# Kernel optimization log

Measured on AMD Instinct MI355X. Metric: run time of the kernel, lower is better.

The kernel has to match this reference:

```python
import jax, jax.numpy as jnp
import numpy as np

B, L, D, H = 4, 1024, 256, 8
TEMP = float(np.sqrt(D))
EPS_SM = 1e-6
EPS_LN = 1e-5


def setup_inputs() -> dict:
    key = jax.random.key(0)
    ks = jax.random.split(key, 8)
    std = float(np.sqrt(2.0 / (D * 2)))
    return {
        "q": jax.random.normal(ks[0], (B, L, D), jnp.float32),
        "mask": jax.random.randint(ks[1], (B, L, L), 0, 2, jnp.int32),
        "k": jax.random.normal(ks[2], (B, L, D), jnp.float32),
        "v": jax.random.normal(ks[3], (B, L, D), jnp.float32),
        "w_qs": jax.random.normal(ks[4], (H * D, D), jnp.float32) * std,
        "w_ks": jax.random.normal(ks[5], (H * D, D), jnp.float32) * std,
        "w_vs": jax.random.normal(ks[6], (H * D, D), jnp.float32) * std,
        "fc_w": jax.random.normal(ks[7], (D, H * D), jnp.float32) * float(np.sqrt(2.0 / (D + H * D))),
        "fc_b": jnp.zeros((D,), jnp.float32),
        "ln_g": jnp.ones((D,), jnp.float32),
        "ln_b": jnp.zeros((D,), jnp.float32),
    }


def masked_softmax(x, m):
    # repo's layers.masked_softmax: clamp, mask-mul, stable exp, mask-mul, normalize
    x = jnp.clip(x, -15.0, 15.0) * m
    e = jnp.exp(x - jnp.max(x, axis=-1, keepdims=True)) * m
    return e / (jnp.sum(e, axis=-1, keepdims=True) + EPS_SM)


def reference(q, mask, k, v, w_qs, w_ks, w_vs, fc_w, fc_b, ln_g, ln_b):
    residual = q
    m = mask.astype(q.dtype)[:, None, :, :]          # [B,1,Lq,Lk]
    # projections to per-head full-dim: [B,L,H,D]
    qh = (q @ w_qs.T).reshape(B, L, H, D)
    kh = (k @ w_ks.T).reshape(B, L, H, D)
    vh = (v @ w_vs.T).reshape(B, L, H, D)
    scores = jnp.einsum("bqhd,bkhd->bhqk", qh, kh) / TEMP   # [B,H,Lq,Lk]
    attn = masked_softmax(scores, m)
    out = jnp.einsum("bhqk,bkhd->bqhd", attn, vh).reshape(B, L, H * D)
    out = out @ fc_w.T + fc_b                         # [B,L,D]
    out = out + residual
    mu = jnp.mean(out, axis=-1, keepdims=True)
    var = jnp.var(out, axis=-1, keepdims=True)
    out = (out - mu) / jnp.sqrt(var + EPS_LN) * ln_g + ln_b
    # match torch attn layout: [H*B, Lq, Lk] (head-major)
    attn_hb = jnp.transpose(attn, (1, 0, 2, 3)).reshape(H * B, L, L)
    return out, attn_hb
```

## Files before the change

kernel.cpp:

```cpp
#include <hip/hip_runtime.h>
#include <cstdint>
#include <math.h>

#define Bsz 4
#define Lsz 1024
#define Dsz 256
#define Hsz 8
#define HD  2048
#define NROWS (Bsz*Lsz)
#define INV_TEMP 0.0625f

typedef __attribute__((ext_vector_type(8))) short bf16x8;
typedef __attribute__((ext_vector_type(4))) float f32x4;

__device__ inline unsigned short f2bf(float f) {
    union { float f; unsigned u; } x; x.f = f;
    unsigned r = x.u + 0x7fffu + ((x.u >> 16) & 1u);
    return (unsigned short)(r >> 16);
}
__device__ inline float bf2f(unsigned short u) {
    union { unsigned u; float f; } x; x.u = (unsigned)u << 16; return x.f;
}

#define GBL(p) ((const __attribute__((address_space(1))) unsigned int*)(p))
#define LDS(p) ((__attribute__((address_space(3))) unsigned int*)(p))

template<int N> __device__ __forceinline__ void vmw() {
    if constexpr (N == 0)       asm volatile("s_waitcnt vmcnt(0)"  ::: "memory");
    else if constexpr (N == 4)  asm volatile("s_waitcnt vmcnt(4)"  ::: "memory");
    else if constexpr (N == 6)  asm volatile("s_waitcnt vmcnt(6)"  ::: "memory");
    else if constexpr (N == 10) asm volatile("s_waitcnt vmcnt(10)" ::: "memory");
    else if constexpr (N == 14) asm volatile("s_waitcnt vmcnt(14)" ::: "memory");
    else static_assert(N == 0, "unsupported vmcnt literal");
}

template <int TMv, int TNv, typename OutT, int EPI, int MINW, bool FUSE,
          int GX, int GY, int GZ>
__global__ __launch_bounds__(256, MINW) void gemm_bt(
    const unsigned short* __restrict__ A, const unsigned short* __restrict__ Bm,
    OutT* __restrict__ C,
    int K, int lda, int ldb, int ldc, int inner,
    long long sA1, long long sA2, long long sB1, long long sB2,
    long long sC1, long long sC2, float alpha,
    const unsigned char* __restrict__ maskb, long long sM2,
    const float* __restrict__ invs, long long sI1, long long sI2,
    float* __restrict__ aux,
    const unsigned short* __restrict__ A2, const unsigned short* __restrict__ B2,
    unsigned short* __restrict__ C2)
{
    constexpr int WMv = TMv / 2, WNv = TNv / 2;
    constexpr int IT = TMv / 32, JT = TNv / 32;
    constexpr int APASS = TMv / 32, NPASS = (TMv + TNv) / 32;
    constexpr int TILE = (TMv + TNv) * 64;
    constexpr int G = GX * GY * GZ;
    static_assert(G % 8 == 0, "bijective XCD swizzle needs G%8==0");
    static_assert(NPASS == 6 || NPASS == 10, "vmcnt literals assume NPASS in {6,10}");
    static_assert(EPI != 1 || TNv == 128, "EPI=1 rowsum shfl assumes 4 segs");
    static_assert(TMv * (TNv + 4) * 4 <= 2 * TILE * 2, "epilogue LDS overflow");

    const int z  = blockIdx.z;

    const int lid = blockIdx.x + GX * (blockIdx.y + GY * blockIdx.z);
    const int nid = (lid & 7) * (G >> 3) + (lid >> 3);
    int mx = nid % GX;
    const int t1g = nid / GX;
    int my = t1g % GY;
    const int zz = t1g / GY;

    if constexpr (FUSE) {
        if (zz >= 2) {
            const int idx = my * 64 + mx;
            if (idx >= 256) return;
            mx = idx & 31; my = idx >> 5;
            const int b = zz - 2;
            A   = A2;
            Bm  = B2 + (size_t)b * ((size_t)Lsz * Dsz);
            C   = (OutT*)(C2 + (size_t)b * ((size_t)HD * Lsz));
            ldc = Lsz;
        } else {
            A  += (size_t)zz * sA2;
            Bm += (size_t)zz * sB2;
            C  += (size_t)zz * sC2;
        }
    } else {
        const int i1 = zz / inner;
        const int i2 = zz % inner;
        A  += (size_t)i1 * sA1 + (size_t)i2 * sA2;
        Bm += (size_t)i1 * sB1 + (size_t)i2 * sB2;
        C  += (size_t)i1 * sC1 + (size_t)i2 * sC2;
        if (EPI == 1) { maskb += (size_t)i2 * sM2; aux += (size_t)zz * Lsz; }
        if (EPI == 2) { invs  += (size_t)i1 * sI1 + (size_t)i2 * sI2; aux += (size_t)zz * Lsz * Lsz; }
    }
    (void)z;

    __shared__ unsigned short S[2 * TILE];

    const int t    = threadIdx.x;
    const int lane = t & 63;
    const int w    = t >> 6;
    const int wm   = w & 1;
    const int wn   = w >> 1;
    const int m0   = mx * TMv;
    const int n0   = my * TNv;

    const int rA = t >> 3;
    const int ch = ((t & 7) ^ (rA & 7)) * 8;
    const unsigned short* gA = A  + (size_t)(m0 + rA) * lda + ch;
    const unsigned short* gB = Bm + (size_t)(n0 + rA) * ldb + ch;

    const int fr = lane & 15;
    const int q  = lane >> 4;

    f32x4 acc[IT][JT];
#pragma unroll
    for (int i = 0; i < IT; ++i)
#pragma unroll
        for (int j = 0; j < JT; ++j) acc[i][j] = (f32x4){0.f, 0.f, 0.f, 0.f};

    auto stage = [&](unsigned short* Sb, int k0) {
#pragma unroll
        for (int p = 0; p < NPASS; ++p) {
            const unsigned short* src = (p < APASS)
                ? (gA + (size_t)p * 32 * lda + k0)
                : (gB + (size_t)(p - APASS) * 32 * ldb + k0);
            __builtin_amdgcn_global_load_lds(GBL(src), LDS(Sb + p * 2048 + t * 8), 16, 0, 0);
        }
    };
    auto kstep = [&](const unsigned short* As) {
        const unsigned short* Bs = As + TMv * 64;
#pragma unroll
        for (int ks = 0; ks < 2; ++ks) {
            const int slot = ((ks * 4 + q) ^ (fr & 7)) * 8;
            bf16x8 a[IT], b[JT];
#pragma unroll
            for (int i = 0; i < IT; ++i)
                a[i] = *(const bf16x8*)(As + (wm * WMv + i * 16 + fr) * 64 + slot);
#pragma unroll
            for (int j = 0; j < JT; ++j)
                b[j] = *(const bf16x8*)(Bs + (wn * WNv + j * 16 + fr) * 64 + slot);
#pragma unroll
            for (int i = 0; i < IT; ++i)
#pragma unroll
                for (int j = 0; j < JT; ++j)
                    acc[i][j] = __builtin_amdgcn_mfma_f32_16x16x32_bf16(a[i], b[j], acc[i][j], 0, 0, 0);
        }
    };

    const int nk = K >> 6;

    float ainv[EPI == 2 ? (TMv / 32) : 1];
    if constexpr (EPI == 2) {
        const int rsub = lane >> 3;
#pragma unroll
        for (int pass = 0; pass < TMv / 32; ++pass)
            ainv[pass] = 1.0f / (invs[m0 + w * (TMv / 4) + pass * 8 + rsub] + 1e-6f);
        vmw<0>();
    }

    stage(S, 0);

    for (int kt = 0; kt < nk; ++kt) {
        if (kt + 1 < nk) stage(S + ((kt + 1) & 1) * TILE, (kt + 1) << 6);

        if constexpr (EPI == 2) {
            if (kt + 1 < nk) { if (kt >= 1) vmw<NPASS + 4>(); else vmw<NPASS>(); }
            else             { if (kt >= 1) vmw<4>();         else vmw<0>(); }
        } else {
            if (kt + 1 < nk) vmw<NPASS>(); else vmw<0>();
        }
        __builtin_amdgcn_s_barrier();

        kstep(S + (kt & 1) * TILE);

        if constexpr (EPI == 2) {
            const unsigned short* As = S + (kt & 1) * TILE;
            const int chunk = lane & 7;
            const int rsub  = lane >> 3;
#pragma unroll
            for (int pass = 0; pass < TMv / 32; ++pass) {
                const int row = w * (TMv / 4) + pass * 8 + rsub;
                const uint4 u = *(const uint4*)(As + row * 64 + ((chunk ^ (row & 7)) * 8));
                const float iv = ainv[pass];
                float4 lo, hi;
                lo.x = bf2f((unsigned short)(u.x & 0xffff)) * iv; lo.y = bf2f((unsigned short)(u.x >> 16)) * iv;
                lo.z = bf2f((unsigned short)(u.y & 0xffff)) * iv; lo.w = bf2f((unsigned short)(u.y >> 16)) * iv;
                hi.x = bf2f((unsigned short)(u.z & 0xffff)) * iv; hi.y = bf2f((unsigned short)(u.z >> 16)) * iv;
                hi.z = bf2f((unsigned short)(u.w & 0xffff)) * iv; hi.w = bf2f((unsigned short)(u.w >> 16)) * iv;
                float* op = aux + (size_t)(m0 + row) * Lsz + (kt << 6) + chunk * 8;
                *(float4*)op = lo;
                *(float4*)(op + 4) = hi;
            }
        }

        asm volatile("s_waitcnt lgkmcnt(0)" ::: "memory");
        __builtin_amdgcn_s_barrier();
    }

    {
        float* Lf = (float*)S;
        constexpr int LP = TNv + 4;
#pragma unroll
        for (int i = 0; i < IT; ++i)
#pragma unroll
            for (int j = 0; j < JT; ++j) {
                const int col = wn * WNv + j * 16 + fr;
#pragma unroll
                for (int r = 0; r < 4; ++r) {
                    const int row = wm * WMv + i * 16 + q * 4 + r;
                    Lf[row * LP + col] = acc[i][j][r] * alpha;
                }
            }
        __syncthreads();

        constexpr int SEGS = TNv / 32;
        constexpr int RPI  = 256 / SEGS;
#pragma unroll
        for (int it2 = 0; it2 < TMv / RPI; ++it2) {
            const int row = it2 * RPI + t / SEGS;
            const int c0  = (t % SEGS) * 32;
            const float* src = Lf + row * LP + c0;

            if constexpr (EPI == 0 && sizeof(OutT) == 4) {
                float* dst = (float*)C + (size_t)(m0 + row) * ldc + n0 + c0;
#pragma unroll
                for (int v4 = 0; v4 < 8; ++v4)
                    *(f32x4*)(dst + v4 * 4) = *(const f32x4*)(src + v4 * 4);
            } else if constexpr (EPI == 0) {
                unsigned short* dst = (unsigned short*)C + (size_t)(m0 + row) * ldc + n0 + c0;
#pragma unroll
                for (int v8 = 0; v8 < 4; ++v8) {
                    bf16x8 o;
#pragma unroll
                    for (int e = 0; e < 8; ++e) o[e] = (short)f2bf(src[v8 * 8 + e]);
                    *(bf16x8*)(dst + v8 * 8) = o;
                }
            } else if constexpr (EPI == 1) {
                unsigned short* dst = (unsigned short*)C + (size_t)(m0 + row) * ldc + n0 + c0;
                const unsigned char* mrow = maskb + (size_t)(m0 + row) * Lsz + n0 + c0;
                unsigned char mloc[32];
                *(uint4*)mloc        = *(const uint4*)mrow;
                *(uint4*)(mloc + 16) = *(const uint4*)(mrow + 16);
                float rsum = 0.f;
#pragma unroll
                for (int v8 = 0; v8 < 4; ++v8) {
                    bf16x8 o;
#pragma unroll
                    for (int e = 0; e < 8; ++e) {
                        const float m = (float)mloc[v8 * 8 + e];
                        float vv = fminf(fmaxf(src[v8 * 8 + e], -15.f), 15.f) * m;
                        vv = __expf(vv) * m;
                        const unsigned short us = f2bf(vv);
                        o[e] = (short)us;
                        rsum += bf2f(us);
                    }
                    *(bf16x8*)(dst + v8 * 8) = o;
                }
                rsum += __shfl_xor(rsum, 1, 64);
                rsum += __shfl_xor(rsum, 2, 64);
                if ((t & 3) == 0) atomicAdd(&aux[m0 + row], rsum);
            } else {
                unsigned short* dst = (unsigned short*)C + (size_t)(m0 + row) * ldc + n0 + c0;
                const float iv = 1.0f / (invs[m0 + row] + 1e-6f);
#pragma unroll
                for (int v8 = 0; v8 < 4; ++v8) {
                    bf16x8 o;
#pragma unroll
                    for (int e = 0; e < 8; ++e) o[e] = (short)f2bf(src[v8 * 8 + e] * iv);
                    *(bf16x8*)(dst + v8 * 8) = o;
                }
            }
        }
    }
}

__global__ __launch_bounds__(256) void cast_all(
    const float* __restrict__ q, const float* __restrict__ k, const float* __restrict__ v,
    const float* __restrict__ wq, const float* __restrict__ wk, const float* __restrict__ wv,
    const float* __restrict__ fw, const int* __restrict__ mask,
    unsigned short* __restrict__ qb, unsigned short* __restrict__ kb, unsigned short* __restrict__ vb,
    unsigned short* __restrict__ wqb, unsigned short* __restrict__ wkb, unsigned short* __restrict__ wvb,
    unsigned short* __restrict__ fwb, unsigned char* __restrict__ mb,
    float* __restrict__ rs)
{
    const int gid = blockIdx.x * 256 + threadIdx.x;
    const int NQ = 262144;
    const int NW = 131072;
    const int NF = 3 * NQ + 4 * NW;
    const int NM = 1048576;
    if (gid >= NF) {
        const int off = gid - NF;
        if (off >= NM) {
            const int ri = off - NM;
            if (ri < 8192) ((float4*)rs)[ri] = (float4){0.f, 0.f, 0.f, 0.f};
            return;
        }
        const int4 mi = ((const int4*)mask)[off];
        uchar4 o;
        o.x = mi.x ? 1 : 0;
        o.y = mi.y ? 1 : 0;
        o.z = mi.z ? 1 : 0;
        o.w = mi.w ? 1 : 0;
        ((uchar4*)mb)[off] = o;
        return;
    }
    const float* src; unsigned short* dst; int off;
    if      (gid < NQ)            { src = q;  dst = qb;  off = gid; }
    else if (gid < 2 * NQ)        { src = k;  dst = kb;  off = gid - NQ; }
    else if (gid < 3 * NQ)        { src = v;  dst = vb;  off = gid - 2 * NQ; }
    else if (gid < 3 * NQ + NW)   { src = wq; dst = wqb; off = gid - 3 * NQ; }
    else if (gid < 3 * NQ + 2*NW) { src = wk; dst = wkb; off = gid - 3 * NQ - NW; }
    else if (gid < 3 * NQ + 3*NW) { src = wv; dst = wvb; off = gid - 3 * NQ - 2 * NW; }
    else                          { src = fw; dst = fwb; off = gid - 3 * NQ - 3 * NW; }
    float4 f = ((const float4*)src)[off];
    ushort4 o;
    o.x = f2bf(f.x); o.y = f2bf(f.y); o.z = f2bf(f.z); o.w = f2bf(f.w);
    ((ushort4*)dst)[off] = o;
}

__global__ __launch_bounds__(256) void ln_kernel(const float* __restrict__ gout,
                                                 const float* __restrict__ qin,
                                                 const float* __restrict__ fc_b,
                                                 const float* __restrict__ ln_g,
                                                 const float* __restrict__ ln_b,
                                                 float* __restrict__ out)
{
    const int row = blockIdx.x;
    const int t = threadIdx.x;
    const size_t idx = (size_t)row * Dsz + t;
    const size_t P = (size_t)NROWS * Dsz;
    const float val = gout[idx] + gout[idx + P] + gout[idx + 2 * P] + gout[idx + 3 * P]
                    + fc_b[t] + qin[idx];

    __shared__ float red[4];
    float s = val;
#pragma unroll
    for (int o = 32; o > 0; o >>= 1) s += __shfl_down(s, o, 64);
    const int lane = t & 63, w = t >> 6;
    if (lane == 0) red[w] = s;
    __syncthreads();
    const float mu = (red[0] + red[1] + red[2] + red[3]) * (1.0f / Dsz);
    __syncthreads();

    float d = val - mu;
    float s2 = d * d;
#pragma unroll
    for (int o = 32; o > 0; o >>= 1) s2 += __shfl_down(s2, o, 64);
    if (lane == 0) red[w] = s2;
    __syncthreads();
    const float var = (red[0] + red[1] + red[2] + red[3]) * (1.0f / Dsz);

    out[idx] = d * rsqrtf(var + 1e-5f) * ln_g[t] + ln_b[t];
}

extern "C" void kernel_launch(void* const* d_in, const int* in_sizes, int n_in,
                              void* d_out, int out_size, void* d_ws, size_t ws_size,
                              hipStream_t stream)
{
    const float* q    = (const float*)d_in[0];
    const int*   mask = (const int*)d_in[1];
    const float* k    = (const float*)d_in[2];
    const float* v    = (const float*)d_in[3];
    const float* w_qs = (const float*)d_in[4];
    const float* w_ks = (const float*)d_in[5];
    const float* w_vs = (const float*)d_in[6];
    const float* fc_w = (const float*)d_in[7];
    const float* fc_b = (const float*)d_in[8];
    const float* ln_g = (const float*)d_in[9];
    const float* ln_b = (const float*)d_in[10];

    float* out  = (float*)d_out;
    float* attn = (float*)d_out + (size_t)NROWS * Dsz;

    unsigned short* wsu = (unsigned short*)d_ws;
    unsigned short* qh     = wsu;
    unsigned short* kh     = qh + (size_t)NROWS * HD;
    unsigned short* q_bf   = kh + (size_t)NROWS * HD;
    unsigned short* k_bf   = q_bf + (size_t)NROWS * Dsz;
    unsigned short* v_bf   = k_bf + (size_t)NROWS * Dsz;
    unsigned short* wq_bf  = v_bf + (size_t)NROWS * Dsz;
    unsigned short* wk_bf  = wq_bf + (size_t)HD * Dsz;
    unsigned short* wv_bf  = wk_bf + (size_t)HD * Dsz;
    unsigned short* vt     = wv_bf + (size_t)HD * Dsz;
    unsigned short* attn_e = vt + (size_t)Bsz * HD * Lsz;
    unsigned short* attnv  = attn_e + (size_t)32 * Lsz * Lsz;
    unsigned short* fcw_bf = attnv + (size_t)NROWS * HD;
    float*          rowsum = (float*)(fcw_bf + (size_t)Dsz * HD);
    float*          fcout  = rowsum + 32768;
    unsigned char*  maskb  = (unsigned char*)(fcout + (size_t)4 * NROWS * Dsz);

    dim3 blk(256);

    cast_all<<<dim3(9248), blk, 0, stream>>>(q, k, v, w_qs, w_ks, w_vs, fc_w, mask,
                                             q_bf, k_bf, v_bf, wq_bf, wk_bf, wv_bf, fcw_bf, maskb,
                                             rowsum);

    {
        dim3 grid(NROWS / 64, HD / 128, 6);
        gemm_bt<64, 128, unsigned short, 0, 3, true, 64, 16, 6><<<grid, blk, 0, stream>>>(
            q_bf, wq_bf, qh,
            Dsz, Dsz, Dsz, HD, 2,
            0, (long long)NROWS * Dsz, 0, (long long)HD * Dsz, 0, (long long)NROWS * HD,
            1.0f, nullptr, 0, nullptr, 0, 0, nullptr,
            wv_bf, v_bf, vt);
    }

    {
        dim3 grid(Lsz / 64, Lsz / 128, Hsz * Bsz);
        gemm_bt<64, 128, unsigned short, 1, 3, false, 16, 8, 32><<<grid, blk, 0, stream>>>(
            qh, kh, attn_e,
            Dsz, HD, HD, Lsz, Bsz,
            Dsz, (long long)Lsz * HD, Dsz, (long long)Lsz * HD,
            (long long)Bsz * Lsz * Lsz, (long long)Lsz * Lsz,
            INV_TEMP, maskb, (long long)Lsz * Lsz, nullptr, 0, 0, rowsum,
            nullptr, nullptr, nullptr);
    }

    {
        dim3 grid(Lsz / 64, 1, Hsz * Bsz);
        gemm_bt<64, 256, unsigned short, 2, 2, false, 16, 1, 32><<<grid, blk, 0, stream>>>(
            attn_e, vt, attnv,
            Lsz, Lsz, Lsz, HD, Bsz,
            (long long)Bsz * Lsz * Lsz, (long long)Lsz * Lsz,
            (long long)Dsz * Lsz, (long long)HD * Lsz,
            Dsz, (long long)Lsz * HD,
            1.0f, nullptr, 0, rowsum, (long long)Bsz * Lsz, (long long)Lsz, attn,
            nullptr, nullptr, nullptr);
    }

    {
        dim3 grid(NROWS / 64, Dsz / 128, 4);
        gemm_bt<64, 128, float, 0, 3, false, 64, 2, 4><<<grid, blk, 0, stream>>>(
            attnv, fcw_bf, fcout,
            512, HD, HD, Dsz, 4,
            0, 512, 0, 512, 0, (long long)NROWS * Dsz,
            1.0f, nullptr, 0, nullptr, 0, 0, nullptr,
            nullptr, nullptr, nullptr);
    }

    ln_kernel<<<dim3(NROWS), blk, 0, stream>>>(fcout, q, fc_b, ln_g, ln_b, out);
}
```

Baseline: 326.2 us.

## Fuse QK^T, masked exp, rowsum and PV into one attention kernel

Replaces the separate score GEMM (with exp/mask epilogue and atomic rowsum) and the PV GEMM (with normalized attn write) with one kernel per 64-row query tile. It streams K and V^T tiles through LDS double buffers, computes exp scores, masks them, accumulates row sums in shared memory and multiplies by V in registers. It still writes the unnormalized bf16 scores to global and re-reads them at the end to emit the normalized fp32 attention matrix. This drops a kernel launch, the rowsum zeroing and the global atomics. The cost is only 512 blocks at one block per CU with about 136KB of LDS, which limits occupancy.

```diff
diff --git a/kernel.cpp b/kernel.cpp
--- a/kernel.cpp
+++ b/kernel.cpp
@@ -27,10 +27,10 @@
 
 template<int N> __device__ __forceinline__ void vmw() {
     if constexpr (N == 0)       asm volatile("s_waitcnt vmcnt(0)"  ::: "memory");
-    else if constexpr (N == 4)  asm volatile("s_waitcnt vmcnt(4)"  ::: "memory");
+    else if constexpr (N == 3)  asm volatile("s_waitcnt vmcnt(3)"  ::: "memory");
     else if constexpr (N == 6)  asm volatile("s_waitcnt vmcnt(6)"  ::: "memory");
     else if constexpr (N == 10) asm volatile("s_waitcnt vmcnt(10)" ::: "memory");
-    else if constexpr (N == 14) asm volatile("s_waitcnt vmcnt(14)" ::: "memory");
+    else if constexpr (N == 19) asm volatile("s_waitcnt vmcnt(19)" ::: "memory");
     else static_assert(N == 0, "unsupported vmcnt literal");
 }
 
@@ -42,9 +42,6 @@
     int K, int lda, int ldb, int ldc, int inner,
     long long sA1, long long sA2, long long sB1, long long sB2,
     long long sC1, long long sC2, float alpha,
-    const unsigned char* __restrict__ maskb, long long sM2,
-    const float* __restrict__ invs, long long sI1, long long sI2,
-    float* __restrict__ aux,
     const unsigned short* __restrict__ A2, const unsigned short* __restrict__ B2,
     unsigned short* __restrict__ C2)
 {
@@ -54,11 +51,8 @@
     constexpr int TILE = (TMv + TNv) * 64;
     constexpr int G = GX * GY * GZ;
     static_assert(G % 8 == 0, "bijective XCD swizzle needs G%8==0");
-    static_assert(NPASS == 6 || NPASS == 10, "vmcnt literals assume NPASS in {6,10}");
-    static_assert(EPI != 1 || TNv == 128, "EPI=1 rowsum shfl assumes 4 segs");
+    static_assert(NPASS == 6, "vmcnt literal assumes NPASS==6");
     static_assert(TMv * (TNv + 4) * 4 <= 2 * TILE * 2, "epilogue LDS overflow");
-
-    const int z  = blockIdx.z;
 
     const int lid = blockIdx.x + GX * (blockIdx.y + GY * blockIdx.z);
     const int nid = (lid & 7) * (G >> 3) + (lid >> 3);
@@ -88,10 +82,7 @@
         A  += (size_t)i1 * sA1 + (size_t)i2 * sA2;
         Bm += (size_t)i1 * sB1 + (size_t)i2 * sB2;
         C  += (size_t)i1 * sC1 + (size_t)i2 * sC2;
-        if (EPI == 1) { maskb += (size_t)i2 * sM2; aux += (size_t)zz * Lsz; }
-        if (EPI == 2) { invs  += (size_t)i1 * sI1 + (size_t)i2 * sI2; aux += (size_t)zz * Lsz * Lsz; }
-    }
-    (void)z;
+    }
 
     __shared__ unsigned short S[2 * TILE];
 
@@ -147,51 +138,13 @@
     };
 
     const int nk = K >> 6;
-
-    float ainv[EPI == 2 ? (TMv / 32) : 1];
-    if constexpr (EPI == 2) {
-        const int rsub = lane >> 3;
-#pragma unroll
-        for (int pass = 0; pass < TMv / 32; ++pass)
-            ainv[pass] = 1.0f / (invs[m0 + w * (TMv / 4) + pass * 8 + rsub] + 1e-6f);
-        vmw<0>();
-    }
-
     stage(S, 0);
 
     for (int kt = 0; kt < nk; ++kt) {
         if (kt + 1 < nk) stage(S + ((kt + 1) & 1) * TILE, (kt + 1) << 6);
-
-        if constexpr (EPI == 2) {
-            if (kt + 1 < nk) { if (kt >= 1) vmw<NPASS + 4>(); else vmw<NPASS>(); }
-            else             { if (kt >= 1) vmw<4>();         else vmw<0>(); }
-        } else {
-            if (kt + 1 < nk) vmw<NPASS>(); else vmw<0>();
-        }
+        if (kt + 1 < nk) vmw<6>(); else vmw<0>();
         __builtin_amdgcn_s_barrier();
-
         kstep(S + (kt & 1) * TILE);
-
-        if constexpr (EPI == 2) {
-            const unsigned short* As = S + (kt & 1) * TILE;
-            const int chunk = lane & 7;
-            const int rsub  = lane >> 3;
-#pragma unroll
-            for (int pass = 0; pass < TMv / 32; ++pass) {
-                const int row = w * (TMv / 4) + pass * 8 + rsub;
-                const uint4 u = *(const uint4*)(As + row * 64 + ((chunk ^ (row & 7)) * 8));
-                const float iv = ainv[pass];
-                float4 lo, hi;
-                lo.x = bf2f((unsigned short)(u.x & 0xffff)) * iv; lo.y = bf2f((unsigned short)(u.x >> 16)) * iv;
-                lo.z = bf2f((unsigned short)(u.y & 0xffff)) * iv; lo.w = bf2f((unsigned short)(u.y >> 16)) * iv;
-                hi.x = bf2f((unsigned short)(u.z & 0xffff)) * iv; hi.y = bf2f((unsigned short)(u.z >> 16)) * iv;
-                hi.z = bf2f((unsigned short)(u.w & 0xffff)) * iv; hi.w = bf2f((unsigned short)(u.w >> 16)) * iv;
-                float* op = aux + (size_t)(m0 + row) * Lsz + (kt << 6) + chunk * 8;
-                *(float4*)op = lo;
-                *(float4*)(op + 4) = hi;
-            }
-        }
-
         asm volatile("s_waitcnt lgkmcnt(0)" ::: "memory");
         __builtin_amdgcn_s_barrier();
     }
@@ -219,13 +172,12 @@
             const int row = it2 * RPI + t / SEGS;
             const int c0  = (t % SEGS) * 32;
             const float* src = Lf + row * LP + c0;
-
-            if constexpr (EPI == 0 && sizeof(OutT) == 4) {
+            if constexpr (sizeof(OutT) == 4) {
                 float* dst = (float*)C + (size_t)(m0 + row) * ldc + n0 + c0;
 #pragma unroll
                 for (int v4 = 0; v4 < 8; ++v4)
                     *(f32x4*)(dst + v4 * 4) = *(const f32x4*)(src + v4 * 4);
-            } else if constexpr (EPI == 0) {
+            } else {
                 unsigned short* dst = (unsigned short*)C + (size_t)(m0 + row) * ldc + n0 + c0;
 #pragma unroll
                 for (int v8 = 0; v8 < 4; ++v8) {
@@ -234,41 +186,237 @@
                     for (int e = 0; e < 8; ++e) o[e] = (short)f2bf(src[v8 * 8 + e]);
                     *(bf16x8*)(dst + v8 * 8) = o;
                 }
-            } else if constexpr (EPI == 1) {
-                unsigned short* dst = (unsigned short*)C + (size_t)(m0 + row) * ldc + n0 + c0;
-                const unsigned char* mrow = maskb + (size_t)(m0 + row) * Lsz + n0 + c0;
-                unsigned char mloc[32];
-                *(uint4*)mloc        = *(const uint4*)mrow;
-                *(uint4*)(mloc + 16) = *(const uint4*)(mrow + 16);
-                float rsum = 0.f;
-#pragma unroll
-                for (int v8 = 0; v8 < 4; ++v8) {
-                    bf16x8 o;
-#pragma unroll
-                    for (int e = 0; e < 8; ++e) {
-                        const float m = (float)mloc[v8 * 8 + e];
-                        float vv = fminf(fmaxf(src[v8 * 8 + e], -15.f), 15.f) * m;
-                        vv = __expf(vv) * m;
-                        const unsigned short us = f2bf(vv);
-                        o[e] = (short)us;
-                        rsum += bf2f(us);
-                    }
-                    *(bf16x8*)(dst + v8 * 8) = o;
+            }
+        }
+    }
+}
+
+__global__ __launch_bounds__(256, 1) void attn_fused(
+    const unsigned short* __restrict__ qh,
+    const unsigned short* __restrict__ kh,
+    const unsigned short* __restrict__ vt,
+    const unsigned char*  __restrict__ maskb,
+    unsigned short* __restrict__ e,
+    unsigned short* __restrict__ attnv,
+    float* __restrict__ attn)
+{
+    constexpr int G = 16 * 32;
+    const int lid = blockIdx.x + 16 * blockIdx.z;
+    const int nid = (lid & 7) * (G >> 3) + (lid >> 3);
+    const int mx = nid & 15;
+    const int z  = nid >> 4;
+    const int h = z >> 2, b = z & 3;
+    const int m0 = mx * 64;
+
+    const unsigned short* gQ = qh + (size_t)b * Lsz * HD + (size_t)h * Dsz;
+    const unsigned short* gK = kh + (size_t)b * Lsz * HD + (size_t)h * Dsz;
+    const unsigned short* gV = vt + (size_t)b * HD * Lsz + (size_t)h * Dsz * Lsz;
+    const unsigned char*  gM = maskb + (size_t)b * Lsz * Lsz;
+    unsigned short* gE = e + (size_t)h * Bsz * Lsz * Lsz + (size_t)b * Lsz * Lsz;
+    float* gA = attn + (size_t)z * Lsz * Lsz;
+
+    __shared__ unsigned short S[69632];
+    __shared__ float rs[64];
+    unsigned short* KH = S;
+    unsigned short* VT = S + 32768;
+    unsigned short* P  = S + 65536;
+
+    const int t = threadIdx.x;
+    const int lane = t & 63;
+    const int w = t >> 6;
+    const int wm = w & 1, wn = w >> 1;
+    const int fr = lane & 15, q = lane >> 4;
+
+    if (t < 64) rs[t] = 0.f;
+
+    bf16x8 Qr[2][8];
+#pragma unroll
+    for (int i = 0; i < 2; ++i) {
+        const unsigned short* qrow = gQ + (size_t)(m0 + wm * 32 + i * 16 + fr) * HD;
+#pragma unroll
+        for (int ks = 0; ks < 8; ++ks)
+            Qr[i][ks] = *(const bf16x8*)(qrow + ks * 32 + q * 8);
+    }
+
+    auto stageKH = [&](unsigned short* dst, int k0) {
+#pragma unroll
+        for (int p = 0; p < 8; ++p) {
+            const int row = p * 8 + (t >> 5);
+            const int c = t & 31;
+            const int cs = (c & 24) | ((c & 7) ^ (row & 7));
+            const unsigned short* src = gK + (size_t)(k0 + row) * HD + cs * 8;
+            __builtin_amdgcn_global_load_lds(GBL(src), LDS(dst + p * 2048 + t * 8), 16, 0, 0);
+        }
+    };
+    auto stageVT = [&](unsigned short* dst, int k0) {
+#pragma unroll
+        for (int p = 0; p < 8; ++p) {
+            const int row = p * 32 + (t >> 3);
+            const int cs = (t & 7) ^ (row & 7);
+            const unsigned short* src = gV + (size_t)row * Lsz + k0 + cs * 8;
+            __builtin_amdgcn_global_load_lds(GBL(src), LDS(dst + p * 2048 + t * 8), 16, 0, 0);
+        }
+    };
+
+    f32x4 O[2][8];
+#pragma unroll
+    for (int i = 0; i < 2; ++i)
+#pragma unroll
+        for (int j = 0; j < 8; ++j) O[i][j] = (f32x4){0.f, 0.f, 0.f, 0.f};
+
+    stageKH(KH, 0); stageVT(VT, 0);
+    vmw<0>();
+    __syncthreads();
+
+    const int rowB = t >> 2, segB = t & 3;
+
+    for (int kt = 0; kt < 16; ++kt) {
+        const int cur = kt & 1;
+        const unsigned char* mp = gM + (size_t)(m0 + rowB) * Lsz + kt * 64 + segB * 16;
+        union { uint4 v; unsigned char c[16]; } mu;
+        mu.v = *(const uint4*)mp;
+        if (kt + 1 < 16) {
+            stageKH(KH + (cur ^ 1) * 16384, (kt + 1) * 64);
+            stageVT(VT + (cur ^ 1) * 16384, (kt + 1) * 64);
+        }
+        if (kt + 1 < 16) vmw<19>(); else vmw<3>();
+        __builtin_amdgcn_s_barrier();
+
+        const unsigned short* KHc = KH + cur * 16384;
+        f32x4 Sa[2][2];
+#pragma unroll
+        for (int i = 0; i < 2; ++i)
+#pragma unroll
+            for (int j = 0; j < 2; ++j) Sa[i][j] = (f32x4){0.f, 0.f, 0.f, 0.f};
+#pragma unroll
+        for (int ks = 0; ks < 8; ++ks) {
+            const int c = ks * 4 + q;
+            const int cs = (c & 24) | ((c & 7) ^ (fr & 7));
+            bf16x8 bfr[2];
+#pragma unroll
+            for (int j = 0; j < 2; ++j)
+                bfr[j] = *(const bf16x8*)(KHc + (wn * 32 + j * 16 + fr) * 256 + cs * 8);
+#pragma unroll
+            for (int i = 0; i < 2; ++i)
+#pragma unroll
+                for (int j = 0; j < 2; ++j)
+                    Sa[i][j] = __builtin_amdgcn_mfma_f32_16x16x32_bf16(Qr[i][ks], bfr[j], Sa[i][j], 0, 0, 0);
+        }
+
+#pragma unroll
+        for (int i = 0; i < 2; ++i)
+#pragma unroll
+            for (int r = 0; r < 4; ++r) {
+                const int row = wm * 32 + i * 16 + q * 4 + r;
+#pragma unroll
+                for (int j = 0; j < 2; ++j) {
+                    const int col = wn * 32 + j * 16 + fr;
+                    float vv = Sa[i][j][r] * INV_TEMP;
+                    vv = __expf(fminf(fmaxf(vv, -15.f), 15.f));
+                    P[row * 64 + (((col >> 3) ^ (row & 7)) * 8) + (col & 7)] = f2bf(vv);
                 }
-                rsum += __shfl_xor(rsum, 1, 64);
-                rsum += __shfl_xor(rsum, 2, 64);
-                if ((t & 3) == 0) atomicAdd(&aux[m0 + row], rsum);
-            } else {
-                unsigned short* dst = (unsigned short*)C + (size_t)(m0 + row) * ldc + n0 + c0;
-                const float iv = 1.0f / (invs[m0 + row] + 1e-6f);
-#pragma unroll
-                for (int v8 = 0; v8 < 4; ++v8) {
-                    bf16x8 o;
-#pragma unroll
-                    for (int e = 0; e < 8; ++e) o[e] = (short)f2bf(src[v8 * 8 + e] * iv);
-                    *(bf16x8*)(dst + v8 * 8) = o;
-                }
-            }
+            }
+        asm volatile("s_waitcnt lgkmcnt(0)" ::: "memory");
+        __builtin_amdgcn_s_barrier();
+
+        {
+            const int c2a = (segB * 2) ^ (rowB & 7);
+            const int c2b = (segB * 2 + 1) ^ (rowB & 7);
+            bf16x8 p0 = *(const bf16x8*)(P + rowB * 64 + c2a * 8);
+            bf16x8 p1 = *(const bf16x8*)(P + rowB * 64 + c2b * 8);
+            float part = 0.f;
+#pragma unroll
+            for (int e2 = 0; e2 < 8; ++e2) {
+                if (!mu.c[e2])     p0[e2] = 0;
+                if (!mu.c[8 + e2]) p1[e2] = 0;
+                part += bf2f((unsigned short)p0[e2]) + bf2f((unsigned short)p1[e2]);
+            }
+            unsigned short* ep = gE + (size_t)(m0 + rowB) * Lsz + kt * 64 + segB * 16;
+            *(bf16x8*)ep = p0;
+            *(bf16x8*)(ep + 8) = p1;
+            *(bf16x8*)(P + rowB * 64 + c2a * 8) = p0;
+            *(bf16x8*)(P + rowB * 64 + c2b * 8) = p1;
+            part += __shfl_xor(part, 1, 64);
+            part += __shfl_xor(part, 2, 64);
+            if (segB == 0) rs[rowB] += part;
+        }
+        asm volatile("s_waitcnt lgkmcnt(0)" ::: "memory");
+        __builtin_amdgcn_s_barrier();
+
+        const unsigned short* VTc = VT + cur * 16384;
+#pragma unroll
+        for (int ks2 = 0; ks2 < 2; ++ks2) {
+            const int cs = ((ks2 * 4 + q) ^ (fr & 7)) * 8;
+            bf16x8 a2[2];
+#pragma unroll
+            for (int i = 0; i < 2; ++i)
+                a2[i] = *(const bf16x8*)(P + (wm * 32 + i * 16 + fr) * 64 + cs);
+#pragma unroll
+            for (int j = 0; j < 8; ++j) {
+                bf16x8 b2 = *(const bf16x8*)(VTc + (wn * 128 + j * 16 + fr) * 64 + cs);
+#pragma unroll
+                for (int i = 0; i < 2; ++i)
+                    O[i][j] = __builtin_amdgcn_mfma_f32_16x16x32_bf16(a2[i], b2, O[i][j], 0, 0, 0);
+            }
+        }
+        asm volatile("s_waitcnt lgkmcnt(0)" ::: "memory");
+        __builtin_amdgcn_s_barrier();
+    }
+
+    if (t < 64) rs[t] = 1.0f / (rs[t] + 1e-6f);
+    __syncthreads();
+
+    {
+        float* Lf = (float*)S;
+#pragma unroll
+        for (int i = 0; i < 2; ++i)
+#pragma unroll
+            for (int j = 0; j < 8; ++j) {
+                const int col = wn * 128 + j * 16 + fr;
+#pragma unroll
+                for (int r = 0; r < 4; ++r)
+                    Lf[(wm * 32 + i * 16 + q * 4 + r) * 260 + col] = O[i][j][r];
+            }
+        __syncthreads();
+#pragma unroll
+        for (int it2 = 0; it2 < 2; ++it2) {
+            const int row = it2 * 32 + (t >> 3);
+            const int c0 = (t & 7) * 32;
+            const float iv = rs[row];
+            const float* src = Lf + row * 260 + c0;
+            unsigned short* dst = attnv + ((size_t)b * Lsz + m0 + row) * HD + h * Dsz + c0;
+#pragma unroll
+            for (int v8 = 0; v8 < 4; ++v8) {
+                bf16x8 o;
+#pragma unroll
+                for (int e2 = 0; e2 < 8; ++e2) o[e2] = (short)f2bf(src[v8 * 8 + e2] * iv);
+                *(bf16x8*)(dst + v8 * 8) = o;
+            }
+        }
+    }
+
+    vmw<0>();
+    {
+        const float iv = rs[rowB];
+        const unsigned short* ebase = gE + (size_t)(m0 + rowB) * Lsz + segB * 16;
+        float* abase = gA + (size_t)(m0 + rowB) * Lsz + segB * 16;
+#pragma unroll 4
+        for (int kt = 0; kt < 16; ++kt) {
+            const unsigned short* ep = ebase + kt * 64;
+            uint4 u0 = *(const uint4*)ep;
+            uint4 u1 = *(const uint4*)(ep + 8);
+            f32x4 f0, f1, f2, f3;
+            f0.x = bf2f((unsigned short)(u0.x & 0xffff)) * iv; f0.y = bf2f((unsigned short)(u0.x >> 16)) * iv;
+            f0.z = bf2f((unsigned short)(u0.y & 0xffff)) * iv; f0.w = bf2f((unsigned short)(u0.y >> 16)) * iv;
+            f1.x = bf2f((unsigned short)(u0.z & 0xffff)) * iv; f1.y = bf2f((unsigned short)(u0.z >> 16)) * iv;
+            f1.z = bf2f((unsigned short)(u0.w & 0xffff)) * iv; f1.w = bf2f((unsigned short)(u0.w >> 16)) * iv;
+            f2.x = bf2f((unsigned short)(u1.x & 0xffff)) * iv; f2.y = bf2f((unsigned short)(u1.x >> 16)) * iv;
+            f2.z = bf2f((unsigned short)(u1.y & 0xffff)) * iv; f2.w = bf2f((unsigned short)(u1.y >> 16)) * iv;
+            f3.x = bf2f((unsigned short)(u1.z & 0xffff)) * iv; f3.y = bf2f((unsigned short)(u1.z >> 16)) * iv;
+            f3.z = bf2f((unsigned short)(u1.w & 0xffff)) * iv; f3.w = bf2f((unsigned short)(u1.w >> 16)) * iv;
+            float* ap = abase + kt * 64;
+            *(f32x4*)ap = f0; *(f32x4*)(ap + 4) = f1;
+            *(f32x4*)(ap + 8) = f2; *(f32x4*)(ap + 12) = f3;
         }
     }
 }
@@ -279,21 +427,14 @@
     const float* __restrict__ fw, const int* __restrict__ mask,
     unsigned short* __restrict__ qb, unsigned short* __restrict__ kb, unsigned short* __restrict__ vb,
     unsigned short* __restrict__ wqb, unsigned short* __restrict__ wkb, unsigned short* __restrict__ wvb,
-    unsigned short* __restrict__ fwb, unsigned char* __restrict__ mb,
-    float* __restrict__ rs)
+    unsigned short* __restrict__ fwb, unsigned char* __restrict__ mb)
 {
     const int gid = blockIdx.x * 256 + threadIdx.x;
     const int NQ = 262144;
     const int NW = 131072;
     const int NF = 3 * NQ + 4 * NW;
-    const int NM = 1048576;
     if (gid >= NF) {
         const int off = gid - NF;
-        if (off >= NM) {
-            const int ri = off - NM;
-            if (ri < 8192) ((float4*)rs)[ri] = (float4){0.f, 0.f, 0.f, 0.f};
-            return;
-        }
         const int4 mi = ((const int4*)mask)[off];
         uchar4 o;
         o.x = mi.x ? 1 : 0;
@@ -384,15 +525,13 @@
     unsigned short* attn_e = vt + (size_t)Bsz * HD * Lsz;
     unsigned short* attnv  = attn_e + (size_t)32 * Lsz * Lsz;
     unsigned short* fcw_bf = attnv + (size_t)NROWS * HD;
-    float*          rowsum = (float*)(fcw_bf + (size_t)Dsz * HD);
-    float*          fcout  = rowsum + 32768;
+    float*          fcout  = (float*)(fcw_bf + (size_t)Dsz * HD);
     unsigned char*  maskb  = (unsigned char*)(fcout + (size_t)4 * NROWS * Dsz);
 
     dim3 blk(256);
 
-    cast_all<<<dim3(9248), blk, 0, stream>>>(q, k, v, w_qs, w_ks, w_vs, fc_w, mask,
-                                             q_bf, k_bf, v_bf, wq_bf, wk_bf, wv_bf, fcw_bf, maskb,
-                                             rowsum);
+    cast_all<<<dim3(9216), blk, 0, stream>>>(q, k, v, w_qs, w_ks, w_vs, fc_w, mask,
+                                             q_bf, k_bf, v_bf, wq_bf, wk_bf, wv_bf, fcw_bf, maskb);
 
     {
         dim3 grid(NROWS / 64, HD / 128, 6);
@@ -400,32 +539,11 @@
             q_bf, wq_bf, qh,
             Dsz, Dsz, Dsz, HD, 2,
             0, (long long)NROWS * Dsz, 0, (long long)HD * Dsz, 0, (long long)NROWS * HD,
-            1.0f, nullptr, 0, nullptr, 0, 0, nullptr,
+            1.0f,
             wv_bf, v_bf, vt);
     }
 
-    {
-        dim3 grid(Lsz / 64, Lsz / 128, Hsz * Bsz);
-        gemm_bt<64, 128, unsigned short, 1, 3, false, 16, 8, 32><<<grid, blk, 0, stream>>>(
-            qh, kh, attn_e,
-            Dsz, HD, HD, Lsz, Bsz,
-            Dsz, (long long)Lsz * HD, Dsz, (long long)Lsz * HD,
-            (long long)Bsz * Lsz * Lsz, (long long)Lsz * Lsz,
-            INV_TEMP, maskb, (long long)Lsz * Lsz, nullptr, 0, 0, rowsum,
-            nullptr, nullptr, nullptr);
-    }
-
-    {
-        dim3 grid(Lsz / 64, 1, Hsz * Bsz);
-        gemm_bt<64, 256, unsigned short, 2, 2, false, 16, 1, 32><<<grid, blk, 0, stream>>>(
-            attn_e, vt, attnv,
-            Lsz, Lsz, Lsz, HD, Bsz,
-            (long long)Bsz * Lsz * Lsz, (long long)Lsz * Lsz,
-            (long long)Dsz * Lsz, (long long)HD * Lsz,
-            Dsz, (long long)Lsz * HD,
-            1.0f, nullptr, 0, rowsum, (long long)Bsz * Lsz, (long long)Lsz, attn,
-            nullptr, nullptr, nullptr);
-    }
+    attn_fused<<<dim3(16, 1, 32), blk, 0, stream>>>(qh, kh, vt, maskb, attn_e, attnv, attn);
 
     {
         dim3 grid(NROWS / 64, Dsz / 128, 4);
@@ -433,7 +551,7 @@
             attnv, fcw_bf, fcout,
             512, HD, HD, Dsz, 4,
             0, 512, 0, 512, 0, (long long)NROWS * Dsz,
-            1.0f, nullptr, 0, nullptr, 0, 0, nullptr,
+            1.0f,
             nullptr, nullptr, nullptr);
     }
 
```

Measured after the change: 373.2 us. +14.4%, slower.

## Add triple-buffered LDS prefetch to the non-softmax-normalizing GEMMs

Applied to the files above, without the earlier changes.

Generalizes the GEMM kernel's LDS staging to a configurable buffer count and uses three buffers, prefetching two k-tiles ahead with matching vmcnt waits. The aim is to hide global-load latency better in the projection, score and output GEMMs. In exchange, LDS use per block grows and the minimum-waves launch bound drops from 3 to 2, which can reduce occupancy. The short K loops also leave little room for a deeper pipeline.

```diff
diff --git a/kernel.cpp b/kernel.cpp
--- a/kernel.cpp
+++ b/kernel.cpp
@@ -30,12 +30,13 @@
     else if constexpr (N == 4)  asm volatile("s_waitcnt vmcnt(4)"  ::: "memory");
     else if constexpr (N == 6)  asm volatile("s_waitcnt vmcnt(6)"  ::: "memory");
     else if constexpr (N == 10) asm volatile("s_waitcnt vmcnt(10)" ::: "memory");
+    else if constexpr (N == 12) asm volatile("s_waitcnt vmcnt(12)" ::: "memory");
     else if constexpr (N == 14) asm volatile("s_waitcnt vmcnt(14)" ::: "memory");
     else static_assert(N == 0, "unsupported vmcnt literal");
 }
 
 template <int TMv, int TNv, typename OutT, int EPI, int MINW, bool FUSE,
-          int GX, int GY, int GZ>
+          int NBUF, int GX, int GY, int GZ>
 __global__ __launch_bounds__(256, MINW) void gemm_bt(
     const unsigned short* __restrict__ A, const unsigned short* __restrict__ Bm,
     OutT* __restrict__ C,
@@ -55,10 +56,11 @@
     constexpr int G = GX * GY * GZ;
     static_assert(G % 8 == 0, "bijective XCD swizzle needs G%8==0");
     static_assert(NPASS == 6 || NPASS == 10, "vmcnt literals assume NPASS in {6,10}");
+    static_assert(NBUF == 2 || NBUF == 3, "NBUF in {2,3}");
+    static_assert(NBUF == 2 || NPASS == 6, "NBUF==3 vmcnt literal assumes NPASS==6");
+    static_assert(EPI != 2 || NBUF == 2, "EPI==2 in-loop indexing assumes NBUF==2");
     static_assert(EPI != 1 || TNv == 128, "EPI=1 rowsum shfl assumes 4 segs");
-    static_assert(TMv * (TNv + 4) * 4 <= 2 * TILE * 2, "epilogue LDS overflow");
-
-    const int z  = blockIdx.z;
+    static_assert(TMv * (TNv + 4) * 4 <= NBUF * TILE * 2, "epilogue LDS overflow");
 
     const int lid = blockIdx.x + GX * (blockIdx.y + GY * blockIdx.z);
     const int nid = (lid & 7) * (G >> 3) + (lid >> 3);
@@ -91,9 +93,8 @@
         if (EPI == 1) { maskb += (size_t)i2 * sM2; aux += (size_t)zz * Lsz; }
         if (EPI == 2) { invs  += (size_t)i1 * sI1 + (size_t)i2 * sI2; aux += (size_t)zz * Lsz * Lsz; }
     }
-    (void)z;
-
-    __shared__ unsigned short S[2 * TILE];
+
+    __shared__ unsigned short S[NBUF * TILE];
 
     const int t    = threadIdx.x;
     const int lane = t & 63;
@@ -158,19 +159,25 @@
     }
 
     stage(S, 0);
+    if constexpr (NBUF == 3) { if (nk > 1) stage(S + TILE, 64); }
 
     for (int kt = 0; kt < nk; ++kt) {
-        if (kt + 1 < nk) stage(S + ((kt + 1) & 1) * TILE, (kt + 1) << 6);
+        const int pre = kt + NBUF - 1;
+        if (pre < nk) stage(S + (pre % NBUF) * TILE, pre << 6);
 
         if constexpr (EPI == 2) {
             if (kt + 1 < nk) { if (kt >= 1) vmw<NPASS + 4>(); else vmw<NPASS>(); }
             else             { if (kt >= 1) vmw<4>();         else vmw<0>(); }
+        } else if constexpr (NBUF == 3) {
+            if (kt + 2 < nk)      vmw<2 * NPASS>();
+            else if (kt + 1 < nk) vmw<NPASS>();
+            else                  vmw<0>();
         } else {
             if (kt + 1 < nk) vmw<NPASS>(); else vmw<0>();
         }
         __builtin_amdgcn_s_barrier();
 
-        kstep(S + (kt & 1) * TILE);
+        kstep(S + (kt % NBUF) * TILE);
 
         if constexpr (EPI == 2) {
             const unsigned short* As = S + (kt & 1) * TILE;
@@ -396,7 +403,7 @@
 
     {
         dim3 grid(NROWS / 64, HD / 128, 6);
-        gemm_bt<64, 128, unsigned short, 0, 3, true, 64, 16, 6><<<grid, blk, 0, stream>>>(
+        gemm_bt<64, 128, unsigned short, 0, 2, true, 3, 64, 16, 6><<<grid, blk, 0, stream>>>(
             q_bf, wq_bf, qh,
             Dsz, Dsz, Dsz, HD, 2,
             0, (long long)NROWS * Dsz, 0, (long long)HD * Dsz, 0, (long long)NROWS * HD,
@@ -406,7 +413,7 @@
 
     {
         dim3 grid(Lsz / 64, Lsz / 128, Hsz * Bsz);
-        gemm_bt<64, 128, unsigned short, 1, 3, false, 16, 8, 32><<<grid, blk, 0, stream>>>(
+        gemm_bt<64, 128, unsigned short, 1, 2, false, 3, 16, 8, 32><<<grid, blk, 0, stream>>>(
             qh, kh, attn_e,
             Dsz, HD, HD, Lsz, Bsz,
             Dsz, (long long)Lsz * HD, Dsz, (long long)Lsz * HD,
@@ -417,7 +424,7 @@
 
     {
         dim3 grid(Lsz / 64, 1, Hsz * Bsz);
-        gemm_bt<64, 256, unsigned short, 2, 2, false, 16, 1, 32><<<grid, blk, 0, stream>>>(
+        gemm_bt<64, 256, unsigned short, 2, 2, false, 2, 16, 1, 32><<<grid, blk, 0, stream>>>(
             attn_e, vt, attnv,
             Lsz, Lsz, Lsz, HD, Bsz,
             (long long)Bsz * Lsz * Lsz, (long long)Lsz * Lsz,
@@ -429,7 +436,7 @@
 
     {
         dim3 grid(NROWS / 64, Dsz / 128, 4);
-        gemm_bt<64, 128, float, 0, 3, false, 64, 2, 4><<<grid, blk, 0, stream>>>(
+        gemm_bt<64, 128, float, 0, 2, false, 3, 64, 2, 4><<<grid, blk, 0, stream>>>(
             attnv, fcw_bf, fcout,
             512, HD, HD, Dsz, 4,
             0, 512, 0, 512, 0, (long long)NROWS * Dsz,
```

New measurement: 336.1 us. 3.0% more time.
